# Optimization experiments

Measured on AMD Instinct MI355X. Metric: run time of the kernel, lower is better.

Reference implementation:

```python
import jax, jax.numpy as jnp
import numpy as np

B, S, H, NH = 8, 1024, 512, 8
HD = H // NH  # 64
ALPHA = 32.0


def setup_inputs() -> dict:
    key = jax.random.key(0)
    ks = jax.random.split(key, 8)
    hidden_states = jax.random.normal(ks[0], (B, S, H), dtype=jnp.float32)
    attention_mask = jnp.zeros((B, 1, 1, S), dtype=jnp.float32)
    rel_2d_pos = jax.random.normal(ks[1], (B, NH, S, S), dtype=jnp.float32)
    scale = 0.02
    Wq = jax.random.normal(ks[2], (H, H), dtype=jnp.float32) * scale
    Wk = jax.random.normal(ks[3], (H, H), dtype=jnp.float32) * scale
    Wv = jax.random.normal(ks[4], (H, H), dtype=jnp.float32) * scale
    bq = jnp.zeros((H,), dtype=jnp.float32)
    bk = jnp.zeros((H,), dtype=jnp.float32)
    bv = jnp.zeros((H,), dtype=jnp.float32)
    return {
        "hidden_states": hidden_states,
        "attention_mask": attention_mask,
        "rel_2d_pos": rel_2d_pos,
        "Wq": Wq, "bq": bq, "Wk": Wk, "bk": bk, "Wv": Wv, "bv": bv,
    }


def cogview_attention(scores, alpha=ALPHA):
    # scores / alpha -> amax -> softmax((s - max) * alpha); faithful to original
    scaled = scores / alpha
    max_value = jnp.max(scaled, axis=-1, keepdims=True)
    return jax.nn.softmax((scaled - max_value) * alpha, axis=-1)


def reference(hidden_states, attention_mask, rel_2d_pos, Wq, bq, Wk, bk, Wv, bv):
    b, s, _ = hidden_states.shape
    def split_heads(x):
        return x.reshape(b, s, NH, HD).transpose(0, 2, 1, 3)  # [B,NH,S,HD]
    q = split_heads(hidden_states @ Wq.T + bq)
    k = split_heads(hidden_states @ Wk.T + bk)
    v = split_heads(hidden_states @ Wv.T + bv)
    scale = 1.0 / jnp.sqrt(jnp.float32(HD))
    scores = jnp.einsum("bhqd,bhkd->bhqk", q * scale, k)
    scores = scores + rel_2d_pos  # spatial 2D relative bias
    scores = scores + attention_mask  # additive mask, broadcast [B,1,1,S]
    probs = cogview_attention(scores)
    ctx = jnp.einsum("bhqk,bhkd->bhqd", probs, v)
    ctx = ctx.transpose(0, 2, 1, 3).reshape(b, s, H)
    return ctx
```

## Files before the change

### kernel.cpp

```cpp
#include <hip/hip_runtime.h>

typedef _Float16 f16x8 __attribute__((ext_vector_type(8)));
typedef _Float16 f16x4 __attribute__((ext_vector_type(4)));
typedef float    f32x4 __attribute__((ext_vector_type(4)));

#define MFMA16(a,b,c) __builtin_amdgcn_mfma_f32_16x16x32_f16((a),(b),(c),0,0,0)

constexpr int Bc  = 8;
constexpr int Sc  = 1024;
constexpr int Hc  = 512;
constexpr int NHc = 8;
constexpr int HDc = 64;

__global__ __launch_bounds__(256) void cvt_f16(
    const float* __restrict__ hs,
    const float* __restrict__ wq, const float* __restrict__ wk,
    const float* __restrict__ wv,
    _Float16* __restrict__ hs16, _Float16* __restrict__ w16)
{
    const size_t i4  = (size_t)blockIdx.x * 256 + threadIdx.x;
    const size_t HS4 = (size_t)Bc * Sc * Hc / 4;
    const size_t W4  = (size_t)Hc * Hc / 4;
    float4 v;
    _Float16* dst;
    if (i4 < HS4) {
        v = ((const float4*)hs)[i4];
        dst = hs16 + i4 * 4;
    } else {
        const size_t j = i4 - HS4;
        const int z = (int)(j / W4);
        const size_t o = j - (size_t)z * W4;
        const float* src = (z == 0) ? wq : (z == 1) ? wk : wv;
        v = ((const float4*)src)[o];
        dst = w16 + j * 4;
    }
    f16x4 h;
    h[0] = (_Float16)v.x; h[1] = (_Float16)v.y;
    h[2] = (_Float16)v.z; h[3] = (_Float16)v.w;
    *(f16x4*)dst = h;
}

__global__ __launch_bounds__(256) void qkv_gemm(
    const _Float16* __restrict__ A,
    const _Float16* __restrict__ Bm,
    const float* __restrict__ bq, const float* __restrict__ bk,
    const float* __restrict__ bv,
    _Float16* __restrict__ qws, _Float16* __restrict__ kws,
    _Float16* __restrict__ vws)
{
    __shared__ __align__(16) _Float16 As[128 * 64];
    __shared__ __align__(16) _Float16 Bs[128 * 64];

    const int m0 = blockIdx.x * 128;
    const int n0 = blockIdx.y * 128;
    const int tid  = threadIdx.x;
    const int lane = tid & 63;
    const int w    = tid >> 6;
    const int l15  = lane & 15;
    const int quad = lane >> 4;
    const int wm   = (w >> 1) * 64;
    const int wn   = (w & 1) * 64;

    f32x4 acc[4][4] = {};

    const int srow = tid >> 3;
    const int scol = (tid & 7) * 8;

    for (int k0 = 0; k0 < 512; k0 += 64) {
        __syncthreads();
#pragma unroll
        for (int j = 0; j < 4; ++j) {
            const _Float16* ga = A  + (size_t)(m0 + srow + 32 * j) * 512 + k0 + scol;
            const _Float16* gb = Bm + (size_t)(n0 + srow + 32 * j) * 512 + k0 + scol;
            __builtin_amdgcn_global_load_lds(
                (const __attribute__((address_space(1))) void*)ga,
                (__attribute__((address_space(3))) void*)(As + tid * 8 + j * 2048),
                16, 0, 0);
            __builtin_amdgcn_global_load_lds(
                (const __attribute__((address_space(1))) void*)gb,
                (__attribute__((address_space(3))) void*)(Bs + tid * 8 + j * 2048),
                16, 0, 0);
        }
        __syncthreads();
#pragma unroll
        for (int ks = 0; ks < 2; ++ks) {
            f16x8 af[4], bf[4];
#pragma unroll
            for (int i = 0; i < 4; ++i) {
                af[i] = *(const f16x8*)&As[(wm + i * 16 + l15) * 64 + ks * 32 + quad * 8];
                bf[i] = *(const f16x8*)&Bs[(wn + i * 16 + l15) * 64 + ks * 32 + quad * 8];
            }
#pragma unroll
            for (int mb = 0; mb < 4; ++mb)
#pragma unroll
                for (int nb = 0; nb < 4; ++nb)
                    acc[mb][nb] = MFMA16(af[mb], bf[nb], acc[mb][nb]);
        }
    }

    const int zsel = n0 >> 9;
    const float* bias = (zsel == 0) ? bq : (zsel == 1) ? bk : bv;
#pragma unroll
    for (int nb = 0; nb < 4; ++nb) {
        const int n  = n0 + wn + nb * 16 + l15;
        const int nn = n & 511;
        const int h  = nn >> 6;
        const int hd = nn & 63;
        const float bvv = bias[nn];
#pragma unroll
        for (int mb = 0; mb < 4; ++mb) {
            const int m = m0 + wm + mb * 16 + quad * 4;
            const int b = m >> 10;
            const int s = m & 1023;
            if (zsel == 2) {
                f16x4 t;
#pragma unroll
                for (int rr = 0; rr < 4; ++rr)
                    t[rr] = (_Float16)(acc[mb][nb][rr] + bvv);
                *(f16x4*)&vws[((size_t)(b * NHc + h) * HDc + hd) * Sc + s] = t;
            } else {
                _Float16* dst = (zsel == 0 ? qws : kws)
                              + ((size_t)(b * NHc + h) * Sc + s) * HDc + hd;
#pragma unroll
                for (int rr = 0; rr < 4; ++rr)
                    dst[(size_t)rr * HDc] = (_Float16)(acc[mb][nb][rr] + bvv);
            }
        }
    }
}

__global__ __launch_bounds__(128, 4) void attn(
    const _Float16* __restrict__ qws, const _Float16* __restrict__ kws,
    const _Float16* __restrict__ vws, const float* __restrict__ rel,
    const float* __restrict__ mask, float* __restrict__ out)
{
    const int qt = blockIdx.x;
    const int bh = blockIdx.y;
    const int b  = bh >> 3;
    const int h  = bh & 7;
    const int tid  = threadIdx.x;
    const int w    = tid >> 6;
    const int lane = tid & 63;
    const int l15  = lane & 15;
    const int quad = lane >> 4;
    const int q0w  = qt * 32 + w * 16;

    __shared__ __align__(16) _Float16 lds_p[2][16][72];

    const _Float16* qh = qws + (size_t)bh * Sc * HDc;
    const _Float16* kh = kws + (size_t)bh * Sc * HDc;
    const _Float16* vh = vws + (size_t)bh * HDc * Sc;
    const float* relh  = rel + (size_t)bh * Sc * Sc;
    const float* maskb = mask + (size_t)b * Sc;

    f16x8 qf0 = *(const f16x8*)(qh + (size_t)(q0w + l15) * HDc + quad * 8);
    f16x8 qf1 = *(const f16x8*)(qh + (size_t)(q0w + l15) * HDc + 32 + quad * 8);

    float m_run[4], l_run[4];
    f32x4 o[4] = {};
#pragma unroll
    for (int rj = 0; rj < 4; ++rj) { m_run[rj] = -1e30f; l_run[rj] = 0.f; }

    const float* relp = relh + (size_t)(q0w + quad * 4) * Sc + l15;

#pragma unroll 2
    for (int kt = 0; kt < 16; ++kt) {
        const int kbase = kt * 64;

        float rb[16];
#pragma unroll
        for (int nb = 0; nb < 4; ++nb)
#pragma unroll
            for (int rj = 0; rj < 4; ++rj)
                rb[nb * 4 + rj] = relp[(size_t)rj * Sc + kbase + nb * 16];

        f16x8 kf0[4], kf1[4];
#pragma unroll
        for (int nb = 0; nb < 4; ++nb) {
            const _Float16* kp = kh + (size_t)(kbase + nb * 16 + l15) * HDc + quad * 8;
            kf0[nb] = *(const f16x8*)kp;
            kf1[nb] = *(const f16x8*)(kp + 32);
        }

        f32x4 sc[4] = {};
#pragma unroll
        for (int nb = 0; nb < 4; ++nb) {
            sc[nb] = MFMA16(qf0, kf0[nb], sc[nb]);
            sc[nb] = MFMA16(qf1, kf1[nb], sc[nb]);
        }

#pragma unroll
        for (int nb = 0; nb < 4; ++nb) {
            const float mk = maskb[kbase + nb * 16 + l15];
#pragma unroll
            for (int rj = 0; rj < 4; ++rj)
                sc[nb][rj] = sc[nb][rj] * 0.125f + rb[nb * 4 + rj] + mk;
        }

#pragma unroll
        for (int rj = 0; rj < 4; ++rj) {
            float mx = fmaxf(fmaxf(sc[0][rj], sc[1][rj]), fmaxf(sc[2][rj], sc[3][rj]));
#pragma unroll
            for (int off = 1; off < 16; off <<= 1) mx = fmaxf(mx, __shfl_xor(mx, off));
            const float mnew  = fmaxf(m_run[rj], mx);
            const float alpha = __expf(m_run[rj] - mnew);
            float rs = 0.f;
#pragma unroll
            for (int nb = 0; nb < 4; ++nb) {
                const float p = __expf(sc[nb][rj] - mnew);
                sc[nb][rj] = p;
                rs += p;
            }
#pragma unroll
            for (int off = 1; off < 16; off <<= 1) rs += __shfl_xor(rs, off);
            m_run[rj] = mnew;
            l_run[rj] = l_run[rj] * alpha + rs;
            o[0][rj] *= alpha; o[1][rj] *= alpha; o[2][rj] *= alpha; o[3][rj] *= alpha;
        }

#pragma unroll
        for (int nb = 0; nb < 4; ++nb)
#pragma unroll
            for (int rj = 0; rj < 4; ++rj)
                lds_p[w][quad * 4 + rj][nb * 16 + l15] = (_Float16)sc[nb][rj];
        f16x8 ap0 = *(const f16x8*)&lds_p[w][l15][quad * 8];
        f16x8 ap1 = *(const f16x8*)&lds_p[w][l15][32 + quad * 8];

#pragma unroll
        for (int nb = 0; nb < 4; ++nb) {
            const _Float16* vp = vh + (size_t)(nb * 16 + l15) * Sc + kbase + quad * 8;
            f16x8 v0 = *(const f16x8*)vp;
            f16x8 v1 = *(const f16x8*)(vp + 32);
            o[nb] = MFMA16(ap0, v0, o[nb]);
            o[nb] = MFMA16(ap1, v1, o[nb]);
        }
    }

#pragma unroll
    for (int rj = 0; rj < 4; ++rj) {
        const float linv = 1.0f / l_run[rj];
        const int qrow = q0w + quad * 4 + rj;
#pragma unroll
        for (int nb = 0; nb < 4; ++nb)
            out[((size_t)(b * Sc + qrow)) * Hc + h * HDc + nb * 16 + l15] =
                o[nb][rj] * linv;
    }
}

extern "C" void kernel_launch(void* const* d_in, const int* in_sizes, int n_in,
                              void* d_out, int out_size, void* d_ws, size_t ws_size,
                              hipStream_t stream) {
    const float* hs   = (const float*)d_in[0];
    const float* mask = (const float*)d_in[1];
    const float* rel  = (const float*)d_in[2];
    const float* Wq   = (const float*)d_in[3];
    const float* bq   = (const float*)d_in[4];
    const float* Wk   = (const float*)d_in[5];
    const float* bk   = (const float*)d_in[6];
    const float* Wv   = (const float*)d_in[7];
    const float* bv   = (const float*)d_in[8];
    float* out = (float*)d_out;

    const size_t elems = (size_t)Bc * Sc * Hc;
    _Float16* hs16 = (_Float16*)d_ws;
    _Float16* w16  = hs16 + elems;
    _Float16* qws  = w16 + (size_t)3 * Hc * Hc;
    _Float16* kws  = qws + elems;
    _Float16* vws  = kws + elems;

    const int cvt_blocks = (int)(((size_t)Bc * Sc * Hc + 3 * Hc * Hc) / 4 / 256);
    cvt_f16<<<cvt_blocks, 256, 0, stream>>>(hs, Wq, Wk, Wv, hs16, w16);
    qkv_gemm<<<dim3(64, 12), 256, 0, stream>>>(hs16, w16, bq, bk, bv,
                                               qws, kws, vws);
    attn<<<dim3(32, 64), 128, 0, stream>>>(qws, kws, vws, rel, mask, out);
}
```

Measured before the change: 486.3 us.

## Software-pipeline rel-bias loads one tile ahead and hoist V loads in attention

Restructures the attention key loop into a manually double-buffered form: the relative-position bias for the next key tile is loaded into a second register array while the current tile is processed, and sched_barriers pin where those loads are issued. V fragments are now loaded at the start of each tile together with K, instead of right before the PV MFMAs. The goal is to hide global-memory latency of the large fp32 rel_2d_pos stream. The extra registers are paid for by lowering the occupancy hint from 4 to 3 blocks per SIMD.

After: 491.1 us. No clear change (+1.0%).

```diff
diff --git a/kernel.cpp b/kernel.cpp
--- a/kernel.cpp
+++ b/kernel.cpp
@@ -129,7 +129,7 @@
     }
 }
 
-__global__ __launch_bounds__(128, 4) void attn(
+__global__ __launch_bounds__(128, 3) void attn(
     const _Float16* __restrict__ qws, const _Float16* __restrict__ kws,
     const _Float16* __restrict__ vws, const float* __restrict__ rel,
     const float* __restrict__ mask, float* __restrict__ out)
@@ -163,78 +163,107 @@
 
     const float* relp = relh + (size_t)(q0w + quad * 4) * Sc + l15;
 
-#pragma unroll 2
-    for (int kt = 0; kt < 16; ++kt) {
-        const int kbase = kt * 64;
-
-        float rb[16];
-#pragma unroll
-        for (int nb = 0; nb < 4; ++nb)
-#pragma unroll
-            for (int rj = 0; rj < 4; ++rj)
-                rb[nb * 4 + rj] = relp[(size_t)rj * Sc + kbase + nb * 16];
-
-        f16x8 kf0[4], kf1[4];
-#pragma unroll
-        for (int nb = 0; nb < 4; ++nb) {
-            const _Float16* kp = kh + (size_t)(kbase + nb * 16 + l15) * HDc + quad * 8;
-            kf0[nb] = *(const f16x8*)kp;
-            kf1[nb] = *(const f16x8*)(kp + 32);
-        }
-
-        f32x4 sc[4] = {};
-#pragma unroll
-        for (int nb = 0; nb < 4; ++nb) {
-            sc[nb] = MFMA16(qf0, kf0[nb], sc[nb]);
-            sc[nb] = MFMA16(qf1, kf1[nb], sc[nb]);
-        }
-
-#pragma unroll
-        for (int nb = 0; nb < 4; ++nb) {
-            const float mk = maskb[kbase + nb * 16 + l15];
-#pragma unroll
-            for (int rj = 0; rj < 4; ++rj)
-                sc[nb][rj] = sc[nb][rj] * 0.125f + rb[nb * 4 + rj] + mk;
-        }
-
-#pragma unroll
-        for (int rj = 0; rj < 4; ++rj) {
-            float mx = fmaxf(fmaxf(sc[0][rj], sc[1][rj]), fmaxf(sc[2][rj], sc[3][rj]));
-#pragma unroll
-            for (int off = 1; off < 16; off <<= 1) mx = fmaxf(mx, __shfl_xor(mx, off));
-            const float mnew  = fmaxf(m_run[rj], mx);
-            const float alpha = __expf(m_run[rj] - mnew);
-            float rs = 0.f;
-#pragma unroll
-            for (int nb = 0; nb < 4; ++nb) {
-                const float p = __expf(sc[nb][rj] - mnew);
-                sc[nb][rj] = p;
-                rs += p;
-            }
-#pragma unroll
-            for (int off = 1; off < 16; off <<= 1) rs += __shfl_xor(rs, off);
-            m_run[rj] = mnew;
-            l_run[rj] = l_run[rj] * alpha + rs;
-            o[0][rj] *= alpha; o[1][rj] *= alpha; o[2][rj] *= alpha; o[3][rj] *= alpha;
-        }
-
-#pragma unroll
-        for (int nb = 0; nb < 4; ++nb)
-#pragma unroll
-            for (int rj = 0; rj < 4; ++rj)
-                lds_p[w][quad * 4 + rj][nb * 16 + l15] = (_Float16)sc[nb][rj];
-        f16x8 ap0 = *(const f16x8*)&lds_p[w][l15][quad * 8];
-        f16x8 ap1 = *(const f16x8*)&lds_p[w][l15][32 + quad * 8];
-
-#pragma unroll
-        for (int nb = 0; nb < 4; ++nb) {
-            const _Float16* vp = vh + (size_t)(nb * 16 + l15) * Sc + kbase + quad * 8;
-            f16x8 v0 = *(const f16x8*)vp;
-            f16x8 v1 = *(const f16x8*)(vp + 32);
-            o[nb] = MFMA16(ap0, v0, o[nb]);
-            o[nb] = MFMA16(ap1, v1, o[nb]);
-        }
-    }
+    float rbA[16], rbB[16];
+#pragma unroll
+    for (int nb = 0; nb < 4; ++nb)
+#pragma unroll
+        for (int rj = 0; rj < 4; ++rj)
+            rbA[nb * 4 + rj] = relp[(size_t)rj * Sc + nb * 16];
+
+#define TILE_BODY(KT, CUR, NXT)                                               \
+    {                                                                         \
+        const int kbase = (KT) * 64;                                          \
+                      \
+        float mk[4];                                                          \
+        _Pragma("unroll")                                                     \
+        for (int nb = 0; nb < 4; ++nb)                                        \
+            mk[nb] = maskb[kbase + nb * 16 + l15];                            \
+        f16x8 kf0[4], kf1[4];                                                 \
+        _Pragma("unroll")                                                     \
+        for (int nb = 0; nb < 4; ++nb) {                                      \
+            const _Float16* kp = kh + (size_t)(kbase + nb * 16 + l15) * HDc   \
+                               + quad * 8;                                    \
+            kf0[nb] = *(const f16x8*)kp;                                      \
+            kf1[nb] = *(const f16x8*)(kp + 32);                               \
+        }                                                                     \
+        f16x8 vf0[4], vf1[4];                                                 \
+        _Pragma("unroll")                                                     \
+        for (int nb = 0; nb < 4; ++nb) {                                      \
+            const _Float16* vp = vh + (size_t)(nb * 16 + l15) * Sc + kbase    \
+                               + quad * 8;                                    \
+            vf0[nb] = *(const f16x8*)vp;                                      \
+            vf1[nb] = *(const f16x8*)(vp + 32);                               \
+        }                                                                     \
+                                                               \
+        f32x4 sc[4] = {};                                                     \
+        _Pragma("unroll")                                                     \
+        for (int nb = 0; nb < 4; ++nb) {                                      \
+            sc[nb] = MFMA16(qf0, kf0[nb], sc[nb]);                            \
+            sc[nb] = MFMA16(qf1, kf1[nb], sc[nb]);                            \
+        }                                                                     \
+        \
+        _Pragma("unroll")                                                     \
+        for (int nb = 0; nb < 4; ++nb)                                        \
+            _Pragma("unroll")                                                 \
+            for (int rj = 0; rj < 4; ++rj)                                    \
+                sc[nb][rj] = sc[nb][rj] * 0.125f + CUR[nb * 4 + rj] + mk[nb]; \
+                      \
+        _Pragma("unroll")                                                     \
+        for (int rj = 0; rj < 4; ++rj) {                                      \
+            float mx = fmaxf(fmaxf(sc[0][rj], sc[1][rj]),                     \
+                             fmaxf(sc[2][rj], sc[3][rj]));                    \
+            _Pragma("unroll")                                                 \
+            for (int off = 1; off < 16; off <<= 1)                            \
+                mx = fmaxf(mx, __shfl_xor(mx, off));                          \
+            const float mnew  = fmaxf(m_run[rj], mx);                         \
+            const float alpha = __expf(m_run[rj] - mnew);                     \
+            float rs = 0.f;                                                   \
+            _Pragma("unroll")                                                 \
+            for (int nb = 0; nb < 4; ++nb) {                                  \
+                const float p = __expf(sc[nb][rj] - mnew);                    \
+                sc[nb][rj] = p;                                               \
+                rs += p;                                                      \
+            }                                                                 \
+            _Pragma("unroll")                                                 \
+            for (int off = 1; off < 16; off <<= 1) rs += __shfl_xor(rs, off); \
+            m_run[rj] = mnew;                                                 \
+            l_run[rj] = l_run[rj] * alpha + rs;                               \
+            o[0][rj] *= alpha; o[1][rj] *= alpha;                             \
+            o[2][rj] *= alpha; o[3][rj] *= alpha;                             \
+        }                                                                     \
+          \
+        __builtin_amdgcn_sched_barrier(0);                                    \
+        if ((KT) < 15) {                                                      \
+            _Pragma("unroll")                                                 \
+            for (int nb = 0; nb < 4; ++nb)                                    \
+                _Pragma("unroll")                                             \
+                for (int rj = 0; rj < 4; ++rj)                                \
+                    NXT[nb * 4 + rj] =                                        \
+                        relp[(size_t)rj * Sc + kbase + 64 + nb * 16];         \
+        }                                                                     \
+        __builtin_amdgcn_sched_barrier(0);                                    \
+                  \
+        _Pragma("unroll")                                                     \
+        for (int nb = 0; nb < 4; ++nb)                                        \
+            _Pragma("unroll")                                                 \
+            for (int rj = 0; rj < 4; ++rj)                                    \
+                lds_p[w][quad * 4 + rj][nb * 16 + l15] =                      \
+                    (_Float16)sc[nb][rj];                                     \
+        f16x8 ap0 = *(const f16x8*)&lds_p[w][l15][quad * 8];                  \
+        f16x8 ap1 = *(const f16x8*)&lds_p[w][l15][32 + quad * 8];             \
+                                           \
+        _Pragma("unroll")                                                     \
+        for (int nb = 0; nb < 4; ++nb) {                                      \
+            o[nb] = MFMA16(ap0, vf0[nb], o[nb]);                              \
+            o[nb] = MFMA16(ap1, vf1[nb], o[nb]);                              \
+        }                                                                     \
+    }
+
+    for (int kt = 0; kt < 16; kt += 2) {
+        TILE_BODY(kt, rbA, rbB)
+        TILE_BODY(kt + 1, rbB, rbA)
+    }
+#undef TILE_BODY
 
 #pragma unroll
     for (int rj = 0; rj < 4; ++rj) {
```

## Add producer wave streaming rel_2d_pos tiles into LDS via async loads

Applied to the files above, without the earlier changes.

Adds a third wavefront per block that acts as a producer, prefetching 32x64 tiles of the rel_2d_pos bias into a 4-slot LDS ring buffer two tiles ahead using global_load_lds. The two compute waves synchronize with it through a block barrier each iteration and read the bias from LDS instead of strided global loads. V fragments are also loaded earlier, alongside K, to hide their latency. The aim is to overlap the dominant bias-streaming traffic with compute. In exchange it adds 32KB of LDS per block and a barrier every iteration, which may lower occupancy.

Result: no change. 490.0 us (+0.8%).

```diff
diff --git a/kernel.cpp b/kernel.cpp
--- a/kernel.cpp
+++ b/kernel.cpp
@@ -129,7 +129,7 @@
     }
 }
 
-__global__ __launch_bounds__(128, 4) void attn(
+__global__ __launch_bounds__(192, 3) void attn(
     const _Float16* __restrict__ qws, const _Float16* __restrict__ kws,
     const _Float16* __restrict__ vws, const float* __restrict__ rel,
     const float* __restrict__ mask, float* __restrict__ out)
@@ -139,12 +139,12 @@
     const int b  = bh >> 3;
     const int h  = bh & 7;
     const int tid  = threadIdx.x;
-    const int w    = tid >> 6;
+    const int wv   = tid >> 6;
     const int lane = tid & 63;
     const int l15  = lane & 15;
     const int quad = lane >> 4;
-    const int q0w  = qt * 32 + w * 16;
-
+
+    __shared__ __align__(16) float    rel_buf[4][32 * 64];
     __shared__ __align__(16) _Float16 lds_p[2][16][72];
 
     const _Float16* qh = qws + (size_t)bh * Sc * HDc;
@@ -152,6 +152,47 @@
     const _Float16* vh = vws + (size_t)bh * HDc * Sc;
     const float* relh  = rel + (size_t)bh * Sc * Sc;
     const float* maskb = mask + (size_t)b * Sc;
+    const int q0 = qt * 32;
+
+    if (wv == 2) {
+        const int prow = lane >> 4;
+        const int pcol = (lane & 15) * 4;
+
+#define ISSUE_TILE(T)                                                         \
+        {                                                                     \
+            _Pragma("unroll")                                                 \
+            for (int g = 0; g < 8; ++g) {                                     \
+                const int R = g * 4 + prow;                                   \
+                const float* src = relh + (size_t)(q0 + R) * Sc               \
+                                 + (T) * 64 + pcol;                           \
+                float* dst = &rel_buf[(T) & 3][g * 256 + lane * 4];           \
+                __builtin_amdgcn_global_load_lds(                             \
+                    (const __attribute__((address_space(1))) void*)src,       \
+                    (__attribute__((address_space(3))) void*)dst, 16, 0, 0);  \
+            }                                                                 \
+        }
+
+        ISSUE_TILE(0)
+        ISSUE_TILE(1)
+        for (int kt = 0; kt < 16; ++kt) {
+            if (kt + 2 < 16) ISSUE_TILE(kt + 2)
+            if (kt <= 13) {
+                asm volatile("s_waitcnt vmcnt(16)" ::: "memory");
+            } else if (kt == 14) {
+                asm volatile("s_waitcnt vmcnt(8)" ::: "memory");
+            } else {
+                asm volatile("s_waitcnt vmcnt(0)" ::: "memory");
+            }
+            __builtin_amdgcn_sched_barrier(0);
+            __builtin_amdgcn_s_barrier();
+            __builtin_amdgcn_sched_barrier(0);
+        }
+#undef ISSUE_TILE
+        return;
+    }
+
+    const int w   = wv;
+    const int q0w = q0 + w * 16;
 
     f16x8 qf0 = *(const f16x8*)(qh + (size_t)(q0w + l15) * HDc + quad * 8);
     f16x8 qf1 = *(const f16x8*)(qh + (size_t)(q0w + l15) * HDc + 32 + quad * 8);
@@ -161,18 +202,26 @@
 #pragma unroll
     for (int rj = 0; rj < 4; ++rj) { m_run[rj] = -1e30f; l_run[rj] = 0.f; }
 
-    const float* relp = relh + (size_t)(q0w + quad * 4) * Sc + l15;
-
-#pragma unroll 2
     for (int kt = 0; kt < 16; ++kt) {
+        __builtin_amdgcn_sched_barrier(0);
+        __builtin_amdgcn_s_barrier();
+        __builtin_amdgcn_sched_barrier(0);
+
         const int kbase = kt * 64;
+        const float* rbuf = rel_buf[kt & 3];
 
         float rb[16];
 #pragma unroll
         for (int nb = 0; nb < 4; ++nb)
 #pragma unroll
             for (int rj = 0; rj < 4; ++rj)
-                rb[nb * 4 + rj] = relp[(size_t)rj * Sc + kbase + nb * 16];
+                rb[nb * 4 + rj] =
+                    rbuf[(w * 16 + quad * 4 + rj) * 64 + nb * 16 + l15];
+
+        float mk[4];
+#pragma unroll
+        for (int nb = 0; nb < 4; ++nb)
+            mk[nb] = maskb[kbase + nb * 16 + l15];
 
         f16x8 kf0[4], kf1[4];
 #pragma unroll
@@ -181,6 +230,13 @@
             kf0[nb] = *(const f16x8*)kp;
             kf1[nb] = *(const f16x8*)(kp + 32);
         }
+        f16x8 vf0[4], vf1[4];
+#pragma unroll
+        for (int nb = 0; nb < 4; ++nb) {
+            const _Float16* vp = vh + (size_t)(nb * 16 + l15) * Sc + kbase + quad * 8;
+            vf0[nb] = *(const f16x8*)vp;
+            vf1[nb] = *(const f16x8*)(vp + 32);
+        }
 
         f32x4 sc[4] = {};
 #pragma unroll
@@ -190,12 +246,10 @@
         }
 
 #pragma unroll
-        for (int nb = 0; nb < 4; ++nb) {
-            const float mk = maskb[kbase + nb * 16 + l15];
+        for (int nb = 0; nb < 4; ++nb)
 #pragma unroll
             for (int rj = 0; rj < 4; ++rj)
-                sc[nb][rj] = sc[nb][rj] * 0.125f + rb[nb * 4 + rj] + mk;
-        }
+                sc[nb][rj] = sc[nb][rj] * 0.125f + rb[nb * 4 + rj] + mk[nb];
 
 #pragma unroll
         for (int rj = 0; rj < 4; ++rj) {
@@ -228,11 +282,8 @@
 
 #pragma unroll
         for (int nb = 0; nb < 4; ++nb) {
-            const _Float16* vp = vh + (size_t)(nb * 16 + l15) * Sc + kbase + quad * 8;
-            f16x8 v0 = *(const f16x8*)vp;
-            f16x8 v1 = *(const f16x8*)(vp + 32);
-            o[nb] = MFMA16(ap0, v0, o[nb]);
-            o[nb] = MFMA16(ap1, v1, o[nb]);
+            o[nb] = MFMA16(ap0, vf0[nb], o[nb]);
+            o[nb] = MFMA16(ap1, vf1[nb], o[nb]);
         }
     }
 
@@ -272,5 +323,5 @@
     cvt_f16<<<cvt_blocks, 256, 0, stream>>>(hs, Wq, Wk, Wv, hs16, w16);
     qkv_gemm<<<dim3(64, 12), 256, 0, stream>>>(hs16, w16, bq, bk, bv,
                                                qws, kws, vws);
-    attn<<<dim3(32, 64), 128, 0, stream>>>(qws, kws, vws, rel, mask, out);
+    attn<<<dim3(32, 64), 192, 0, stream>>>(qws, kws, vws, rel, mask, out);
 }
```

## Prefetch rel bias with coalesced float4 loads via LDS and software-pipeline V loads

Applied to the files above, without the earlier changes.

Each lane now reads the relative-position bias as row-contiguous float4s instead of strided scalar loads, then transposes it through a small LDS buffer into the MFMA accumulator layout. The next tile's bias is prefetched into registers while the current tile is computed, and V fragments are loaded before the softmax so their latency overlaps it. Scheduling barriers pin this ordering. The kernel is bound by reading the large fp32 bias tensor, so coalesced, early-issued loads should raise achieved bandwidth, at the cost of more registers and LDS and a loop that is no longer unrolled.

New measurement: 560.2 us. 15.2% more time.

```diff
diff --git a/kernel.cpp b/kernel.cpp
--- a/kernel.cpp
+++ b/kernel.cpp
@@ -145,6 +145,7 @@
     const int quad = lane >> 4;
     const int q0w  = qt * 32 + w * 16;
 
+    __shared__ __align__(16) float    rel_lds[2][16][68];
     __shared__ __align__(16) _Float16 lds_p[2][16][72];
 
     const _Float16* qh = qws + (size_t)bh * Sc * HDc;
@@ -153,6 +154,13 @@
     const float* relh  = rel + (size_t)bh * Sc * Sc;
     const float* maskb = mask + (size_t)b * Sc;
 
+    const float* relp = relh + (size_t)(q0w + l15) * Sc + quad * 4;
+
+    float4 rl[4];
+#pragma unroll
+    for (int g = 0; g < 4; ++g)
+        rl[g] = *(const float4*)(relp + g * 16);
+
     f16x8 qf0 = *(const f16x8*)(qh + (size_t)(q0w + l15) * HDc + quad * 8);
     f16x8 qf1 = *(const f16x8*)(qh + (size_t)(q0w + l15) * HDc + 32 + quad * 8);
 
@@ -161,19 +169,19 @@
 #pragma unroll
     for (int rj = 0; rj < 4; ++rj) { m_run[rj] = -1e30f; l_run[rj] = 0.f; }
 
-    const float* relp = relh + (size_t)(q0w + quad * 4) * Sc + l15;
-
-#pragma unroll 2
+#pragma unroll 1
     for (int kt = 0; kt < 16; ++kt) {
         const int kbase = kt * 64;
 
-        float rb[16];
-#pragma unroll
-        for (int nb = 0; nb < 4; ++nb)
-#pragma unroll
-            for (int rj = 0; rj < 4; ++rj)
-                rb[nb * 4 + rj] = relp[(size_t)rj * Sc + kbase + nb * 16];
-
+#pragma unroll
+        for (int g = 0; g < 4; ++g)
+            *(float4*)&rel_lds[w][l15][quad * 4 + g * 16] = rl[g];
+        __builtin_amdgcn_sched_barrier(0);
+
+        float mk[4];
+#pragma unroll
+        for (int nb = 0; nb < 4; ++nb)
+            mk[nb] = maskb[kbase + nb * 16 + l15];
         f16x8 kf0[4], kf1[4];
 #pragma unroll
         for (int nb = 0; nb < 4; ++nb) {
@@ -181,6 +189,7 @@
             kf0[nb] = *(const f16x8*)kp;
             kf1[nb] = *(const f16x8*)(kp + 32);
         }
+        __builtin_amdgcn_sched_barrier(0);
 
         f32x4 sc[4] = {};
 #pragma unroll
@@ -188,14 +197,35 @@
             sc[nb] = MFMA16(qf0, kf0[nb], sc[nb]);
             sc[nb] = MFMA16(qf1, kf1[nb], sc[nb]);
         }
-
+        __builtin_amdgcn_sched_barrier(0);
+
+        f16x8 vf0[4], vf1[4];
 #pragma unroll
         for (int nb = 0; nb < 4; ++nb) {
-            const float mk = maskb[kbase + nb * 16 + l15];
+            const _Float16* vp = vh + (size_t)(nb * 16 + l15) * Sc + kbase + quad * 8;
+            vf0[nb] = *(const f16x8*)vp;
+            vf1[nb] = *(const f16x8*)(vp + 32);
+        }
+
+        if (kt < 15) {
+#pragma unroll
+            for (int g = 0; g < 4; ++g)
+                rl[g] = *(const float4*)(relp + kbase + 64 + g * 16);
+        }
+        __builtin_amdgcn_sched_barrier(0);
+
+        float rb[16];
+#pragma unroll
+        for (int nb = 0; nb < 4; ++nb)
 #pragma unroll
             for (int rj = 0; rj < 4; ++rj)
-                sc[nb][rj] = sc[nb][rj] * 0.125f + rb[nb * 4 + rj] + mk;
-        }
+                rb[nb * 4 + rj] = rel_lds[w][quad * 4 + rj][nb * 16 + l15];
+
+#pragma unroll
+        for (int nb = 0; nb < 4; ++nb)
+#pragma unroll
+            for (int rj = 0; rj < 4; ++rj)
+                sc[nb][rj] = sc[nb][rj] * 0.125f + rb[nb * 4 + rj] + mk[nb];
 
 #pragma unroll
         for (int rj = 0; rj < 4; ++rj) {
@@ -228,11 +258,8 @@
 
 #pragma unroll
         for (int nb = 0; nb < 4; ++nb) {
-            const _Float16* vp = vh + (size_t)(nb * 16 + l15) * Sc + kbase + quad * 8;
-            f16x8 v0 = *(const f16x8*)vp;
-            f16x8 v1 = *(const f16x8*)(vp + 32);
-            o[nb] = MFMA16(ap0, v0, o[nb]);
-            o[nb] = MFMA16(ap1, v1, o[nb]);
+            o[nb] = MFMA16(ap0, vf0[nb], o[nb]);
+            o[nb] = MFMA16(ap1, vf1[nb], o[nb]);
         }
     }
 
```
